# Performance work log

Hardware: AMD Instinct MI355X
Metric: run time of the kernel (lower is better)

## Reference

```python
import jax, jax.numpy as jnp
import numpy as np

B, T, F, S = 32, 2048, 256, 256  # batch, time, features, state_size
W_SCALE = 0.02  # keeps the linear recurrence spectrally stable over T steps


def setup_inputs() -> dict:
    key = jax.random.key(0)
    k1, k2, k3 = jax.random.split(key, 3)
    inputs = jax.random.normal(k1, (B, T, F), dtype=jnp.float32)
    W = jax.random.normal(k2, (S + F, S), dtype=jnp.float32) * W_SCALE
    b = jax.random.normal(k3, (S,), dtype=jnp.float32) * 0.01
    return {"inputs": inputs, "W": W, "b": b}


def reference(inputs, W, b):
    # state_t = Dense(concat(state_{t-1}, obs_t)) -- linear recurrence over time.
    def step(state, x_t):
        new_state = jnp.concatenate([state, x_t], axis=-1) @ W + b  # [B, S]
        return new_state, new_state

    state0 = jnp.zeros((inputs.shape[0], W.shape[1]), dtype=inputs.dtype)
    xs = jnp.swapaxes(inputs, 0, 1)  # [T, B, F] for scan over time
    final_state, outs = jax.lax.scan(step, state0, xs)
    outputs = jnp.swapaxes(outs, 0, 1)  # [B, T, S]
    return outputs, final_state
```

## Files before the change

kernel.cpp:

```cpp
#include <hip/hip_runtime.h>
#include <hip/hip_bf16.h>


#define B_DIM 32
#define T_DIM 2048
#define F_DIM 256
#define S_DIM 256

#define L_CHUNK 16
#define WARM    16
#define NCHUNK  (T_DIM / L_CHUNK)
#define ROWS    16
#define LDS_STRIDE 264
#define XL_STRIDE 40

typedef __bf16 bf16x8 __attribute__((ext_vector_type(8)));
typedef __bf16 bf16x4 __attribute__((ext_vector_type(4)));
typedef float  f32x4  __attribute__((ext_vector_type(4)));

#define MFMA(a, b, c) __builtin_amdgcn_mfma_f32_16x16x32_bf16((a), (b), (c), 0, 0, 0)

__device__ __forceinline__ void barrier_lds() {
    asm volatile("s_waitcnt lgkmcnt(0)" ::: "memory");
    __builtin_amdgcn_s_barrier();
    asm volatile("" ::: "memory");
}


#define WF_ELEMS (256 * 64 * 8)

__global__ __launch_bounds__(64)
void pack_w_kernel(const float* __restrict__ Wm, __bf16* __restrict__ WF)
{
    const int b    = blockIdx.x;
    const int sel  = b >> 7;
    const int cg   = (b >> 3) & 15;
    const int kt   = b & 7;
    const int lane = threadIdx.x;
    const int q    = lane >> 4;
    const int m16  = lane & 15;

    const float* src = Wm + (size_t)(sel * 256 + kt * 32 + q * 8) * S_DIM + cg * 16 + m16;
    bf16x8 w;
    #pragma unroll
    for (int j = 0; j < 8; ++j)
        w[j] = (__bf16)src[(size_t)j * S_DIM];
    *(bf16x8*)(WF + ((size_t)b * 64 + lane) * 8) = w;
}

__global__ __launch_bounds__(256, 2)
void compute_u_kernel(const float* __restrict__ X,
                      const __bf16* __restrict__ WF,
                      const float* __restrict__ bv,
                      __bf16* __restrict__ U)
{
    __shared__ __align__(16) __bf16 xl[2][8 * 16 * XL_STRIDE];

    const int tid  = threadIdx.x;
    const int wave = tid >> 6;
    const int lane = tid & 63;
    const int m16  = lane & 15;
    const int q    = lane >> 4;

    const int srow = tid >> 4;
    const int scid = tid & 15;
    const int skt  = scid >> 1;
    const int soff = (scid & 1) * 16;

    const __bf16* WxF = WF + 128 * 64 * 8;
    bf16x8 wx[8][4];
    #pragma unroll
    for (int kt = 0; kt < 8; ++kt)
        #pragma unroll
        for (int c = 0; c < 4; ++c)
            wx[kt][c] = *(const bf16x8*)(WxF + (((size_t)(wave * 4 + c) * 8 + kt) * 64 + lane) * 8);

    f32x4 bb[4];
    #pragma unroll
    for (int c = 0; c < 4; ++c)
        bb[c] = *(const f32x4*)(bv + (wave * 4 + c) * 16 + q * 4);

    const int tau0 = blockIdx.x * 8;

    f32x4 xr[4];
    {
        const int t = tau0 >> 1, half = tau0 & 1;
        const float* xp = X + ((size_t)(half * 16 + srow) * T_DIM + t) * F_DIM + scid * 16;
        #pragma unroll
        for (int j = 0; j < 4; ++j) xr[j] = ((const f32x4*)xp)[j];
    }
    {
        __bf16* dst = &xl[0][(skt * 16 + srow) * XL_STRIDE + soff];
        bf16x8 v0, v1;
        #pragma unroll
        for (int j = 0; j < 4; ++j) {
            v0[j] = (__bf16)xr[0][j]; v0[4 + j] = (__bf16)xr[1][j];
            v1[j] = (__bf16)xr[2][j]; v1[4 + j] = (__bf16)xr[3][j];
        }
        *(bf16x8*)dst = v0; *(bf16x8*)(dst + 8) = v1;
    }
    barrier_lds();

    for (int i = 0; i < 8; ++i) {
        const int tau = tau0 + i;

        if (i < 7) {
            const int t1 = (tau + 1) >> 1, h1 = (tau + 1) & 1;
            const float* xp = X + ((size_t)(h1 * 16 + srow) * T_DIM + t1) * F_DIM + scid * 16;
            #pragma unroll
            for (int j = 0; j < 4; ++j) xr[j] = ((const f32x4*)xp)[j];
        }

        bf16x8 xa[8];
        const __bf16* rb = &xl[i & 1][0];
        #pragma unroll
        for (int kt = 0; kt < 8; ++kt)
            xa[kt] = *(const bf16x8*)(rb + (kt * 16 + m16) * XL_STRIDE + q * 8);

        f32x4 acc[4];
        #pragma unroll
        for (int c = 0; c < 4; ++c)
            acc[c] = bb[c];
        #pragma unroll
        for (int kt = 0; kt < 8; ++kt)
            #pragma unroll
            for (int c = 0; c < 4; ++c)
                acc[c] = MFMA(wx[kt][c], xa[kt], acc[c]);

        __bf16* up = U + ((size_t)(tau * 4 + wave) * 64 + lane) * 16;
        bf16x8 p0, p1;
        #pragma unroll
        for (int j = 0; j < 8; ++j) {
            p0[j] = (__bf16)acc[j >> 2][j & 3];
            p1[j] = (__bf16)acc[2 + (j >> 2)][j & 3];
        }
        *(bf16x8*)up       = p0;
        *(bf16x8*)(up + 8) = p1;

        if (i < 7) {
            __bf16* dst = &xl[(i + 1) & 1][(skt * 16 + srow) * XL_STRIDE + soff];
            bf16x8 v0, v1;
            #pragma unroll
            for (int j = 0; j < 4; ++j) {
                v0[j] = (__bf16)xr[0][j]; v0[4 + j] = (__bf16)xr[1][j];
                v1[j] = (__bf16)xr[2][j]; v1[4 + j] = (__bf16)xr[3][j];
            }
            *(bf16x8*)dst = v0; *(bf16x8*)(dst + 8) = v1;
            barrier_lds();
        }
    }
}

__global__ __launch_bounds__(256, 1)
void scan_kernel(const __bf16* __restrict__ U,
                 const __bf16* __restrict__ WF,
                 float* __restrict__ out)
{
    __shared__ __align__(16) __bf16 sbuf[2][ROWS * LDS_STRIDE];

    const int tid  = threadIdx.x;
    const int wave = tid >> 6;
    const int lane = tid & 63;
    const int m16  = lane & 15;
    const int q    = lane >> 4;

    const int chunk   = blockIdx.x >> 1;
    const int half    = blockIdx.x & 1;
    const int rowbase = half * 16;

    {
        int* z = (int*)&sbuf[0][0];
        const int nints = (2 * ROWS * LDS_STRIDE) / 2;
        for (int i = tid; i < nints; i += 256) z[i] = 0;
    }

    bf16x8 ws[8][4];
    #pragma unroll
    for (int kt = 0; kt < 8; ++kt)
        #pragma unroll
        for (int c = 0; c < 4; ++c)
            ws[kt][c] = *(const bf16x8*)(WF + (((size_t)(wave * 4 + c) * 8 + kt) * 64 + lane) * 8);

    barrier_lds();

    const int t0 = chunk * L_CHUNK;
    const int tb = (t0 >= WARM) ? (t0 - WARM) : 0;
    const int te = t0 + L_CHUNK;

    auto uptr = [&](int t) {
        return U + ((size_t)((t * 2 + half) * 4 + wave) * 64 + lane) * 16;
    };

    bf16x8 uA0, uA1, uB0, uB1;
    {
        const __bf16* p = uptr(tb);
        uA0 = *(const bf16x8*)p; uA1 = *(const bf16x8*)(p + 8);
    }
    {
        const __bf16* p = uptr(tb + 1);
        uB0 = *(const bf16x8*)p; uB1 = *(const bf16x8*)(p + 8);
    }

    int bufc = 0;

    auto step = [&](int t, bf16x8& cu0, bf16x8& cu1) {
        f32x4 accA[4], accB[4];
        #pragma unroll
        for (int r = 0; r < 4; ++r) {
            accA[0][r] = (float)cu0[r];
            accA[1][r] = (float)cu0[4 + r];
            accA[2][r] = (float)cu1[r];
            accA[3][r] = (float)cu1[4 + r];
        }
        #pragma unroll
        for (int c = 0; c < 4; ++c)
            accB[c] = (f32x4){0.f, 0.f, 0.f, 0.f};

        if (t + 2 < te) {
            const __bf16* np = uptr(t + 2);
            cu0 = *(const bf16x8*)np;
            cu1 = *(const bf16x8*)(np + 8);
        }

        bf16x8 sa[8];
        const __bf16* sb = &sbuf[bufc][m16 * LDS_STRIDE + q * 8];
        #pragma unroll
        for (int kt = 0; kt < 8; ++kt)
            sa[kt] = *(const bf16x8*)(sb + kt * 32);

        #pragma unroll
        for (int kt = 0; kt < 4; ++kt)
            #pragma unroll
            for (int c = 0; c < 4; ++c)
                accA[c] = MFMA(ws[kt][c], sa[kt], accA[c]);
        #pragma unroll
        for (int kt = 4; kt < 8; ++kt)
            #pragma unroll
            for (int c = 0; c < 4; ++c)
                accB[c] = MFMA(ws[kt][c], sa[kt], accB[c]);

        __bf16* wb = &sbuf[bufc ^ 1][0];
        #pragma unroll
        for (int c = 0; c < 4; ++c) {
            f32x4 a = accA[c] + accB[c];
            bf16x4 v;
            #pragma unroll
            for (int r = 0; r < 4; ++r) v[r] = (__bf16)a[r];
            *(bf16x4*)(&wb[m16 * LDS_STRIDE + wave * 64 + c * 16 + q * 4]) = v;
        }

        barrier_lds();

        if (t >= t0) {
            const int row = tid >> 4;
            const int c0  = (tid & 15) * 16;
            const __bf16* sp = &sbuf[bufc ^ 1][row * LDS_STRIDE + c0];
            bf16x8 v0 = *(const bf16x8*)sp;
            bf16x8 v1 = *(const bf16x8*)(sp + 8);
            float* op = out + ((size_t)(rowbase + row) * T_DIM + t) * S_DIM + c0;
            f32x4 o0, o1, o2, o3;
            #pragma unroll
            for (int j = 0; j < 4; ++j) {
                o0[j] = (float)v0[j];
                o1[j] = (float)v0[4 + j];
                o2[j] = (float)v1[j];
                o3[j] = (float)v1[4 + j];
            }
            *(f32x4*)(op)      = o0;
            *(f32x4*)(op + 4)  = o1;
            *(f32x4*)(op + 8)  = o2;
            *(f32x4*)(op + 12) = o3;
        }
        if (chunk == NCHUNK - 1 && t == T_DIM - 1) {
            const int row = tid >> 4;
            const int c0  = (tid & 15) * 16;
            const __bf16* sp = &sbuf[bufc ^ 1][row * LDS_STRIDE + c0];
            bf16x8 v0 = *(const bf16x8*)sp;
            bf16x8 v1 = *(const bf16x8*)(sp + 8);
            float* op = out + (size_t)B_DIM * T_DIM * S_DIM + (size_t)(rowbase + row) * S_DIM + c0;
            #pragma unroll
            for (int j = 0; j < 8; ++j) {
                op[j]     = (float)v0[j];
                op[8 + j] = (float)v1[j];
            }
        }
        bufc ^= 1;
    };

    for (int t = tb; t < te; t += 2) {
        step(t,     uA0, uA1);
        step(t + 1, uB0, uB1);
    }
}

extern "C" void kernel_launch(void* const* d_in, const int* in_sizes, int n_in,
                              void* d_out, int out_size, void* d_ws, size_t ws_size,
                              hipStream_t stream) {
    const float* X  = (const float*)d_in[0];
    const float* Wm = (const float*)d_in[1];
    const float* bv = (const float*)d_in[2];
    float* out = (float*)d_out;

    __bf16* U  = (__bf16*)d_ws;
    __bf16* WF = (__bf16*)d_ws + (size_t)4096 * 4 * 64 * 16;

    pack_w_kernel<<<dim3(256), dim3(64), 0, stream>>>(Wm, WF);
    compute_u_kernel<<<dim3(512), dim3(256), 0, stream>>>(X, WF, bv, U);
    scan_kernel<<<dim3(NCHUNK * 2), dim3(256), 0, stream>>>(U, WF, out);
}
```

Measured before the change: 162.4 us.

## Process both batch halves per block and halve scan chunk length

Each scan block now handles all 32 batch rows as two interleaved 16-row groups, so the register-resident W fragments are reused for two independent MFMA chains per step. This hides MFMA dependency latency, where before accumulation was split into two partial sums. The chunk length drops from 16 to 8, which keeps the block count at 256. It also means the 16-step warm-up is now twice the useful length, so redundant recompute per output rises, and each step carries twice the LDS traffic and register pressure.

```diff
diff --git a/kernel.cpp b/kernel.cpp
--- a/kernel.cpp
+++ b/kernel.cpp
@@ -7,7 +7,7 @@
 #define F_DIM 256
 #define S_DIM 256
 
-#define L_CHUNK 16
+#define L_CHUNK 8
 #define WARM    16
 #define NCHUNK  (T_DIM / L_CHUNK)
 #define ROWS    16
@@ -156,7 +156,7 @@
                  const __bf16* __restrict__ WF,
                  float* __restrict__ out)
 {
-    __shared__ __align__(16) __bf16 sbuf[2][ROWS * LDS_STRIDE];
+    __shared__ __align__(16) __bf16 sbuf[2][2][ROWS * LDS_STRIDE];
 
     const int tid  = threadIdx.x;
     const int wave = tid >> 6;
@@ -164,13 +164,11 @@
     const int m16  = lane & 15;
     const int q    = lane >> 4;
 
-    const int chunk   = blockIdx.x >> 1;
-    const int half    = blockIdx.x & 1;
-    const int rowbase = half * 16;
+    const int chunk = blockIdx.x;
 
     {
-        int* z = (int*)&sbuf[0][0];
-        const int nints = (2 * ROWS * LDS_STRIDE) / 2;
+        int* z = (int*)&sbuf[0][0][0];
+        const int nints = (2 * 2 * ROWS * LDS_STRIDE) / 2;
         for (int i = tid; i < nints; i += 256) z[i] = 0;
     }
 
@@ -187,66 +185,69 @@
     const int tb = (t0 >= WARM) ? (t0 - WARM) : 0;
     const int te = t0 + L_CHUNK;
 
-    auto uptr = [&](int t) {
-        return U + ((size_t)((t * 2 + half) * 4 + wave) * 64 + lane) * 16;
+    auto uptr = [&](int t, int h) {
+        return U + ((size_t)((t * 2 + h) * 4 + wave) * 64 + lane) * 16;
     };
 
-    bf16x8 uA0, uA1, uB0, uB1;
+    bf16x8 uE00, uE01, uE10, uE11;
+    bf16x8 uO00, uO01, uO10, uO11;
     {
-        const __bf16* p = uptr(tb);
-        uA0 = *(const bf16x8*)p; uA1 = *(const bf16x8*)(p + 8);
-    }
-    {
-        const __bf16* p = uptr(tb + 1);
-        uB0 = *(const bf16x8*)p; uB1 = *(const bf16x8*)(p + 8);
+        const __bf16* p = uptr(tb, 0);     uE00 = *(const bf16x8*)p; uE01 = *(const bf16x8*)(p + 8);
+        const __bf16* r = uptr(tb, 1);     uE10 = *(const bf16x8*)r; uE11 = *(const bf16x8*)(r + 8);
+        const __bf16* s = uptr(tb + 1, 0); uO00 = *(const bf16x8*)s; uO01 = *(const bf16x8*)(s + 8);
+        const __bf16* w = uptr(tb + 1, 1); uO10 = *(const bf16x8*)w; uO11 = *(const bf16x8*)(w + 8);
     }
 
     int bufc = 0;
 
-    auto step = [&](int t, bf16x8& cu0, bf16x8& cu1) {
-        f32x4 accA[4], accB[4];
+    auto step = [&](int t, bf16x8& a0, bf16x8& a1, bf16x8& b0, bf16x8& b1) {
+        f32x4 acc0[4], acc1[4];
         #pragma unroll
         for (int r = 0; r < 4; ++r) {
-            accA[0][r] = (float)cu0[r];
-            accA[1][r] = (float)cu0[4 + r];
-            accA[2][r] = (float)cu1[r];
-            accA[3][r] = (float)cu1[4 + r];
-        }
-        #pragma unroll
-        for (int c = 0; c < 4; ++c)
-            accB[c] = (f32x4){0.f, 0.f, 0.f, 0.f};
+            acc0[0][r] = (float)a0[r];
+            acc0[1][r] = (float)a0[4 + r];
+            acc0[2][r] = (float)a1[r];
+            acc0[3][r] = (float)a1[4 + r];
+            acc1[0][r] = (float)b0[r];
+            acc1[1][r] = (float)b0[4 + r];
+            acc1[2][r] = (float)b1[r];
+            acc1[3][r] = (float)b1[4 + r];
+        }
 
         if (t + 2 < te) {
-            const __bf16* np = uptr(t + 2);
-            cu0 = *(const bf16x8*)np;
-            cu1 = *(const bf16x8*)(np + 8);
-        }
-
-        bf16x8 sa[8];
-        const __bf16* sb = &sbuf[bufc][m16 * LDS_STRIDE + q * 8];
-        #pragma unroll
-        for (int kt = 0; kt < 8; ++kt)
-            sa[kt] = *(const bf16x8*)(sb + kt * 32);
-
-        #pragma unroll
-        for (int kt = 0; kt < 4; ++kt)
+            const __bf16* p = uptr(t + 2, 0);
+            a0 = *(const bf16x8*)p; a1 = *(const bf16x8*)(p + 8);
+            const __bf16* r = uptr(t + 2, 1);
+            b0 = *(const bf16x8*)r; b1 = *(const bf16x8*)(r + 8);
+        }
+
+        bf16x8 sa0[8], sa1[8];
+        const __bf16* sb0 = &sbuf[bufc][0][m16 * LDS_STRIDE + q * 8];
+        const __bf16* sb1 = &sbuf[bufc][1][m16 * LDS_STRIDE + q * 8];
+        #pragma unroll
+        for (int kt = 0; kt < 8; ++kt) {
+            sa0[kt] = *(const bf16x8*)(sb0 + kt * 32);
+            sa1[kt] = *(const bf16x8*)(sb1 + kt * 32);
+        }
+
+        #pragma unroll
+        for (int kt = 0; kt < 8; ++kt) {
             #pragma unroll
             for (int c = 0; c < 4; ++c)
-                accA[c] = MFMA(ws[kt][c], sa[kt], accA[c]);
-        #pragma unroll
-        for (int kt = 4; kt < 8; ++kt)
+                acc0[c] = MFMA(ws[kt][c], sa0[kt], acc0[c]);
             #pragma unroll
             for (int c = 0; c < 4; ++c)
-                accB[c] = MFMA(ws[kt][c], sa[kt], accB[c]);
-
-        __bf16* wb = &sbuf[bufc ^ 1][0];
+                acc1[c] = MFMA(ws[kt][c], sa1[kt], acc1[c]);
+        }
+
         #pragma unroll
         for (int c = 0; c < 4; ++c) {
-            f32x4 a = accA[c] + accB[c];
-            bf16x4 v;
-            #pragma unroll
-            for (int r = 0; r < 4; ++r) v[r] = (__bf16)a[r];
-            *(bf16x4*)(&wb[m16 * LDS_STRIDE + wave * 64 + c * 16 + q * 4]) = v;
+            bf16x4 v0, v1;
+            #pragma unroll
+            for (int r = 0; r < 4; ++r) { v0[r] = (__bf16)acc0[c][r]; v1[r] = (__bf16)acc1[c][r]; }
+            const int off = m16 * LDS_STRIDE + wave * 64 + c * 16 + q * 4;
+            *(bf16x4*)(&sbuf[bufc ^ 1][0][off]) = v0;
+            *(bf16x4*)(&sbuf[bufc ^ 1][1][off]) = v1;
         }
 
         barrier_lds();
@@ -254,42 +255,48 @@
         if (t >= t0) {
             const int row = tid >> 4;
             const int c0  = (tid & 15) * 16;
-            const __bf16* sp = &sbuf[bufc ^ 1][row * LDS_STRIDE + c0];
-            bf16x8 v0 = *(const bf16x8*)sp;
-            bf16x8 v1 = *(const bf16x8*)(sp + 8);
-            float* op = out + ((size_t)(rowbase + row) * T_DIM + t) * S_DIM + c0;
-            f32x4 o0, o1, o2, o3;
-            #pragma unroll
-            for (int j = 0; j < 4; ++j) {
-                o0[j] = (float)v0[j];
-                o1[j] = (float)v0[4 + j];
-                o2[j] = (float)v1[j];
-                o3[j] = (float)v1[4 + j];
+            #pragma unroll
+            for (int h = 0; h < 2; ++h) {
+                const __bf16* sp = &sbuf[bufc ^ 1][h][row * LDS_STRIDE + c0];
+                bf16x8 v0 = *(const bf16x8*)sp;
+                bf16x8 v1 = *(const bf16x8*)(sp + 8);
+                float* op = out + ((size_t)(h * 16 + row) * T_DIM + t) * S_DIM + c0;
+                f32x4 o0, o1, o2, o3;
+                #pragma unroll
+                for (int j = 0; j < 4; ++j) {
+                    o0[j] = (float)v0[j];
+                    o1[j] = (float)v0[4 + j];
+                    o2[j] = (float)v1[j];
+                    o3[j] = (float)v1[4 + j];
+                }
+                *(f32x4*)(op)      = o0;
+                *(f32x4*)(op + 4)  = o1;
+                *(f32x4*)(op + 8)  = o2;
+                *(f32x4*)(op + 12) = o3;
             }
-            *(f32x4*)(op)      = o0;
-            *(f32x4*)(op + 4)  = o1;
-            *(f32x4*)(op + 8)  = o2;
-            *(f32x4*)(op + 12) = o3;
         }
         if (chunk == NCHUNK - 1 && t == T_DIM - 1) {
             const int row = tid >> 4;
             const int c0  = (tid & 15) * 16;
-            const __bf16* sp = &sbuf[bufc ^ 1][row * LDS_STRIDE + c0];
-            bf16x8 v0 = *(const bf16x8*)sp;
-            bf16x8 v1 = *(const bf16x8*)(sp + 8);
-            float* op = out + (size_t)B_DIM * T_DIM * S_DIM + (size_t)(rowbase + row) * S_DIM + c0;
-            #pragma unroll
-            for (int j = 0; j < 8; ++j) {
-                op[j]     = (float)v0[j];
-                op[8 + j] = (float)v1[j];
+            #pragma unroll
+            for (int h = 0; h < 2; ++h) {
+                const __bf16* sp = &sbuf[bufc ^ 1][h][row * LDS_STRIDE + c0];
+                bf16x8 v0 = *(const bf16x8*)sp;
+                bf16x8 v1 = *(const bf16x8*)(sp + 8);
+                float* op = out + (size_t)B_DIM * T_DIM * S_DIM + (size_t)(h * 16 + row) * S_DIM + c0;
+                #pragma unroll
+                for (int j = 0; j < 8; ++j) {
+                    op[j]     = (float)v0[j];
+                    op[8 + j] = (float)v1[j];
+                }
             }
         }
         bufc ^= 1;
     };
 
     for (int t = tb; t < te; t += 2) {
-        step(t,     uA0, uA1);
-        step(t + 1, uB0, uB1);
+        step(t,     uE00, uE01, uE10, uE11);
+        step(t + 1, uO00, uO01, uO10, uO11);
     }
 }
 
@@ -306,5 +313,5 @@
 
     pack_w_kernel<<<dim3(256), dim3(64), 0, stream>>>(Wm, WF);
     compute_u_kernel<<<dim3(512), dim3(256), 0, stream>>>(X, WF, bv, U);
-    scan_kernel<<<dim3(NCHUNK * 2), dim3(256), 0, stream>>>(U, WF, out);
-}
+    scan_kernel<<<dim3(NCHUNK), dim3(256), 0, stream>>>(U, WF, out);
+}
```

Measured after the change: 164.0 us. About the same (+1.0%).
